# Performance work log

Measured on AMD Instinct MI355X. Metric: run time of the kernel, lower is better.

The kernel has to match this reference:

```python
import jax, jax.numpy as jnp
import numpy as np

B, C, H, W = 16, 512, 64, 64
K = 5  # k_size for channel=512: int(abs((log2(512)+1)/2)) = 5, already odd


def setup_inputs() -> dict:
    key = jax.random.key(0)
    k1, k2, k3, k4 = jax.random.split(key, 4)
    x = jax.random.normal(k1, (B, C, H, W), dtype=jnp.float32)
    w1x1 = jax.random.normal(k2, (C, C), dtype=jnp.float32) * (1.0 / np.sqrt(C))
    b1x1 = jax.random.normal(k3, (C,), dtype=jnp.float32) * 0.01
    w1d = jax.random.normal(k4, (C, K), dtype=jnp.float32) * (1.0 / np.sqrt(K))
    return {"x": x, "w1x1": w1x1, "b1x1": b1x1, "w1d": w1d}


def reference(x, w1x1, b1x1, w1d):
    b, c, h, w = x.shape
    # conv1x1 (pointwise) + softmax over all c*h*w elements per batch.
    # NOTE: y is computed but unused in the original module's return; kept for fidelity.
    y = jnp.einsum('bchw,oc->bohw', x, w1x1) + b1x1[None, :, None, None]
    y = jax.nn.softmax(y.reshape(b, -1), axis=1).reshape(b, c, h, w)
    del y
    # channel attention: global average pool -> per-channel conv1d on a length-1 slice.
    z = x.mean(axis=(2, 3))  # (b, c)
    k = w1d.shape[1]
    center = (k - 1) // 2
    # Each Conv1d sees a zero-padded length-k window with z_i at the center tap,
    # so out_i = sum_j W_i[j] * pad(z_i)[j] = W_i[center] * z_i. Implement the
    # full dot against the padded window (identical math, vectorized over channels).
    zpad = jnp.zeros((b, c, k), dtype=x.dtype).at[:, :, center].set(z)
    zc = jnp.einsum('bck,ck->bc', zpad, w1d)
    gate = jax.nn.sigmoid(zc)[:, :, None, None]  # (b, c, 1, 1)
    return x * gate
```

## Files before the change

kernel.cpp:

```cpp
#include <hip/hip_runtime.h>


#define NC 512
#define HW 4096
#define PER_LANE 16

typedef float vf4 __attribute__((ext_vector_type(4)));

__global__ __launch_bounds__(256) void mcanet_gate_kernel(
    const float* __restrict__ x,
    const float* __restrict__ w1d,
    float* __restrict__ out)
{
    const int wave  = threadIdx.x >> 6;
    const int lane  = threadIdx.x & 63;
    const int plane = (blockIdx.x << 2) + wave;
    const int c = plane & (NC - 1);

    const float wc = w1d[c * 5 + 2];

    const long long base = (long long)plane * HW;
    const vf4* __restrict__ xin = (const vf4*)(x + base);
    vf4* __restrict__ o = (vf4*)(out + base);

    vf4 v[PER_LANE];
    #pragma unroll
    for (int i = 0; i < PER_LANE; ++i)
        v[i] = xin[lane + (i << 6)];

    vf4 acc = v[0];
    #pragma unroll
    for (int i = 1; i < PER_LANE; ++i)
        acc += v[i];
    float s = (acc.x + acc.y) + (acc.z + acc.w);

    #pragma unroll
    for (int off = 32; off > 0; off >>= 1)
        s += __shfl_xor(s, off, 64);

    const float zc = wc * (s * (1.0f / (float)HW));
    const float g  = 1.0f / (1.0f + __expf(-zc));

    #pragma unroll
    for (int i = 0; i < PER_LANE; ++i) {
        vf4 r = v[i] * g;
        o[lane + (i << 6)] = r;
    }
}

extern "C" void kernel_launch(void* const* d_in, const int* in_sizes, int n_in,
                              void* d_out, int out_size, void* d_ws, size_t ws_size,
                              hipStream_t stream) {
    const float* x   = (const float*)d_in[0];
    const float* w1d = (const float*)d_in[3];
    float* out = (float*)d_out;

    const int planes = 16 * NC;
    mcanet_gate_kernel<<<planes / 4, 256, 0, stream>>>(x, w1d, out);
}
```

Measured before the change: 237.5 us.

## Process four planes per wave with software-pipelined nontemporal loads

Launches a fixed grid where each wave handles four channel planes, issuing loads for the next plane before finishing reduction and scaling of the current one, using three register buffers. Loads and stores use nontemporal hints to avoid cache pollution for streaming data. The aim is to keep more memory requests in flight per wave and cut launch/tail overhead. It risks higher register pressure and lower occupancy.

```diff
diff --git a/kernel.cpp b/kernel.cpp
--- a/kernel.cpp
+++ b/kernel.cpp
@@ -4,6 +4,9 @@
 #define NC 512
 #define HW 4096
 #define PER_LANE 16
+#define NBLK 512
+#define NWAVE (NBLK * 4)
+#define PPW 4
 
 typedef float vf4 __attribute__((ext_vector_type(4)));
 
@@ -12,40 +15,56 @@
     const float* __restrict__ w1d,
     float* __restrict__ out)
 {
-    const int wave  = threadIdx.x >> 6;
-    const int lane  = threadIdx.x & 63;
-    const int plane = (blockIdx.x << 2) + wave;
-    const int c = plane & (NC - 1);
+    const int lane = threadIdx.x & 63;
+    const int gw   = (blockIdx.x << 2) + (threadIdx.x >> 6);
 
-    const float wc = w1d[c * 5 + 2];
+    vf4 va[PER_LANE], vb[PER_LANE], vc[PER_LANE];
 
-    const long long base = (long long)plane * HW;
-    const vf4* __restrict__ xin = (const vf4*)(x + base);
-    vf4* __restrict__ o = (vf4*)(out + base);
+#define ISSUE(buf, pl)                                                        \
+    do {                                                                      \
+        const vf4* __restrict__ xin_ =                                        \
+            (const vf4*)(x + (long long)(pl) * HW);                           \
+        _Pragma("unroll")                                                     \
+        for (int i_ = 0; i_ < PER_LANE; ++i_)                                 \
+            buf[i_] = __builtin_nontemporal_load(xin_ + lane + (i_ << 6));    \
+    } while (0)
 
-    vf4 v[PER_LANE];
-    #pragma unroll
-    for (int i = 0; i < PER_LANE; ++i)
-        v[i] = xin[lane + (i << 6)];
+#define FINISH(buf, pl)                                                       \
+    do {                                                                      \
+        vf4 acc_ = buf[0];                                                    \
+        _Pragma("unroll")                                                     \
+        for (int i_ = 1; i_ < PER_LANE; ++i_) acc_ += buf[i_];                \
+        float s_ = (acc_.x + acc_.y) + (acc_.z + acc_.w);                     \
+        _Pragma("unroll")                                                     \
+        for (int off_ = 32; off_ > 0; off_ >>= 1)                             \
+            s_ += __shfl_xor(s_, off_, 64);                                   \
+        const float wc_ = w1d[((pl) & (NC - 1)) * 5 + 2];                     \
+        const float zc_ = wc_ * (s_ * (1.0f / (float)HW));                    \
+        const float g_  = 1.0f / (1.0f + __expf(-zc_));                       \
+        vf4* __restrict__ o_ = (vf4*)(out + (long long)(pl) * HW);            \
+        _Pragma("unroll")                                                     \
+        for (int i_ = 0; i_ < PER_LANE; ++i_) {                               \
+            vf4 r_ = buf[i_] * g_;                                            \
+            __builtin_nontemporal_store(r_, o_ + lane + (i_ << 6));           \
+        }                                                                     \
+    } while (0)
 
-    vf4 acc = v[0];
-    #pragma unroll
-    for (int i = 1; i < PER_LANE; ++i)
-        acc += v[i];
-    float s = (acc.x + acc.y) + (acc.z + acc.w);
+    const int p0 = gw;
+    const int p1 = gw + NWAVE;
+    const int p2 = gw + 2 * NWAVE;
+    const int p3 = gw + 3 * NWAVE;
 
-    #pragma unroll
-    for (int off = 32; off > 0; off >>= 1)
-        s += __shfl_xor(s, off, 64);
+    ISSUE(va, p0);
+    ISSUE(vb, p1);
+    FINISH(va, p0);
+    ISSUE(vc, p2);
+    FINISH(vb, p1);
+    ISSUE(va, p3);
+    FINISH(vc, p2);
+    FINISH(va, p3);
 
-    const float zc = wc * (s * (1.0f / (float)HW));
-    const float g  = 1.0f / (1.0f + __expf(-zc));
-
-    #pragma unroll
-    for (int i = 0; i < PER_LANE; ++i) {
-        vf4 r = v[i] * g;
-        o[lane + (i << 6)] = r;
-    }
+#undef ISSUE
+#undef FINISH
 }
 
 extern "C" void kernel_launch(void* const* d_in, const int* in_sizes, int n_in,
@@ -55,6 +74,5 @@
     const float* w1d = (const float*)d_in[3];
     float* out = (float*)d_out;
 
-    const int planes = 16 * NC;
-    mcanet_gate_kernel<<<planes / 4, 256, 0, stream>>>(x, w1d, out);
+    mcanet_gate_kernel<<<NBLK, 256, 0, stream>>>(x, w1d, out);
 }
```

Result: faster. 227.3 us (-4.3%).
